# Optimization experiments

Measured on AMD Instinct MI355X. Metric: run time of the kernel, lower is better.

## Reference

```python
import jax, jax.numpy as jnp
import numpy as np

N = 100000
E = 1600000
IN_C = 128
HID = 32
HEADS = 4
NUM_CLASSES = 16
NEG_SLOPE = 0.2


def setup_inputs() -> dict:
    key = jax.random.key(0)
    ks = jax.random.split(key, 10)
    x = jax.random.normal(ks[0], (N, IN_C), dtype=jnp.float32)
    edge_index = jax.random.randint(ks[1], (2, E), 0, N, dtype=jnp.int32)
    s1 = 1.0 / np.sqrt(IN_C)
    s2 = 1.0 / np.sqrt(HID * HEADS)
    W1 = jax.random.normal(ks[2], (IN_C, HEADS * HID), dtype=jnp.float32) * s1
    att_src1 = jax.random.normal(ks[3], (HEADS, HID), dtype=jnp.float32) * s1
    att_dst1 = jax.random.normal(ks[4], (HEADS, HID), dtype=jnp.float32) * s1
    b1 = jnp.zeros((HEADS * HID,), dtype=jnp.float32)
    W2 = jax.random.normal(ks[5], (HEADS * HID, NUM_CLASSES), dtype=jnp.float32) * s2
    att_src2 = jax.random.normal(ks[6], (1, NUM_CLASSES), dtype=jnp.float32) * s2
    att_dst2 = jax.random.normal(ks[7], (1, NUM_CLASSES), dtype=jnp.float32) * s2
    b2 = jnp.zeros((NUM_CLASSES,), dtype=jnp.float32)
    return {"x": x, "edge_index": edge_index,
            "W1": W1, "att_src1": att_src1, "att_dst1": att_dst1, "b1": b1,
            "W2": W2, "att_src2": att_src2, "att_dst2": att_dst2, "b2": b2}


def _gat_conv(x, src, dst, W, att_src, att_dst, b):
    # PyG GATConv: shared linear for src/dst, additive attention, segment softmax over dst.
    n = x.shape[0]
    H, C = att_src.shape
    h = (x @ W).reshape(n, H, C)                       # [N, H, C]
    a_s = jnp.einsum('nhc,hc->nh', h, att_src)          # [N, H]
    a_d = jnp.einsum('nhc,hc->nh', h, att_dst)          # [N, H]
    e = a_s[src] + a_d[dst]                             # [E, H]
    e = jnp.where(e >= 0, e, NEG_SLOPE * e)             # leaky_relu(0.2)
    # numerically stable segment softmax over destination node groups
    e_max = jax.ops.segment_max(e, dst, num_segments=n)
    e_exp = jnp.exp(e - e_max[dst])
    denom = jax.ops.segment_sum(e_exp, dst, num_segments=n)
    alpha = e_exp / denom[dst]                          # [E, H]
    msg = h[src] * alpha[:, :, None]                    # [E, H, C]
    out = jax.ops.segment_sum(msg, dst, num_segments=n) # [N, H, C]
    return out.reshape(n, H * C) + b


def reference(x, edge_index, W1, att_src1, att_dst1, b1, W2, att_src2, att_dst2, b2):
    n = x.shape[0]
    # add_self_loops=True (PyG default), same augmented edge set for both layers
    loop = jnp.arange(n, dtype=edge_index.dtype)
    src = jnp.concatenate([edge_index[0], loop])
    dst = jnp.concatenate([edge_index[1], loop])
    h = _gat_conv(x, src, dst, W1, att_src1, att_dst1, b1)
    h = jax.nn.elu(h)
    out = _gat_conv(h, src, dst, W2, att_src2, att_dst2, b2)
    return out
```

## Files before the change

### kernel.cpp

```cpp
#include <hip/hip_runtime.h>
#include <hip/hip_bf16.h>
#include <math.h>


typedef unsigned short u16;
typedef unsigned int u32;
typedef __attribute__((ext_vector_type(8))) short bf16x8;
typedef __attribute__((ext_vector_type(4))) float f32x4;

__device__ __forceinline__ float eluf(float v) { return v > 0.f ? v : expm1f(v); }
__device__ __forceinline__ u16 f2bf(float f) {
    u32 u = __float_as_uint(f);
    u += 0x7fff + ((u >> 16) & 1);
    return (u16)(u >> 16);
}
__device__ __forceinline__ float bf2f(u16 u) {
    return __uint_as_float(((u32)u) << 16);
}
__device__ __forceinline__ float expleaky(float e) {
    float m = e >= 0.f ? 1.44269504f : 0.28853901f;
    return exp2f(e * m);
}

__global__ __launch_bounds__(256) void ksetup(
    const float* __restrict__ W1, const float* __restrict__ W2,
    const float* __restrict__ ats2, const float* __restrict__ atd2,
    u16* __restrict__ w1fh, u16* __restrict__ w1fl,
    float* __restrict__ u, float* __restrict__ v, u16* __restrict__ w2tb,
    int* __restrict__ deg, int N)
{
    const int b = blockIdx.x, tid = threadIdx.x;
    if (b < 64) {
        int idx = b * 256 + tid;
        int j = idx & 7, l = (idx >> 3) & 63, q = (idx >> 9) & 3, ct = idx >> 11;
        int k = q * 32 + (l >> 4) * 8 + j;
        int n = ct * 16 + (l & 15);
        float w = W1[k * 128 + n];
        u16 hv = f2bf(w);
        w1fh[idx] = hv;
        w1fl[idx] = f2bf(w - bf2f(hv));
    } else if (b == 64) {
        if (tid < 128) {
            float su = 0.f, sv = 0.f;
            #pragma unroll
            for (int j = 0; j < 16; ++j) {
                float w = W2[tid * 16 + j];
                su = fmaf(w, ats2[j], su);
                sv = fmaf(w, atd2[j], sv);
                w2tb[j * 128 + tid] = f2bf(w);
            }
            u[tid] = su; v[tid] = sv;
        }
    } else {
        int z = (b - 65) * 1024 + tid * 4;
        if (z < N) *(int4*)&deg[z] = make_int4(0, 0, 0, 0);
    }
}

__global__ __launch_bounds__(256) void khist(
    const int* __restrict__ ei, int* __restrict__ deg, int* __restrict__ rank,
    int E)
{
    const int base = blockIdx.x * 2048 + threadIdx.x;
    int dd[8];
    #pragma unroll
    for (int k = 0; k < 8; ++k) {
        int e = base + 256 * k;
        dd[k] = (e < E) ? ei[E + e] : -1;
    }
    int rk[8];
    #pragma unroll
    for (int k = 0; k < 8; ++k)
        if (dd[k] >= 0) rk[k] = atomicAdd(&deg[dd[k]], 1);
    #pragma unroll
    for (int k = 0; k < 8; ++k) {
        int e = base + 256 * k;
        if (e < E) rank[e] = rk[k];
    }
}

#define REPW 40
__global__ __launch_bounds__(256) void kgemm(
    const float* __restrict__ x, const u16* __restrict__ w1fh,
    const u16* __restrict__ w1fl,
    const float* __restrict__ att_s, const float* __restrict__ att_d,
    u16* __restrict__ h1b, float* __restrict__ as1, float* __restrict__ ad1,
    int N, int GB)
{
    __shared__ u16 rep[4][16 * REPW];
    const int tid = threadIdx.x;
    const int wv = tid >> 6, lane = tid & 63;
    const int m = lane & 15, quad = lane >> 4;
    const int h = wv;

    bf16x8 bh[2][4], bl[2][4];
    #pragma unroll
    for (int sub = 0; sub < 2; ++sub) {
        #pragma unroll
        for (int q = 0; q < 4; ++q) {
            const int off = (((2 * h + sub) * 4 + q) * 64 + lane) * 8;
            bh[sub][q] = *(const bf16x8*)&w1fh[off];
            bl[sub][q] = *(const bf16x8*)&w1fl[off];
        }
    }
    #pragma unroll
    for (int sub = 0; sub < 2; ++sub) {
        #pragma unroll
        for (int q = 0; q < 4; ++q) {
            asm volatile("" : "+v"(bh[sub][q]));
            asm volatile("" : "+v"(bl[sub][q]));
        }
    }

    const float cs0 = att_s[h * 32 + m];
    const float cs1 = att_s[h * 32 + 16 + m];
    const float cd0 = att_d[h * 32 + m];
    const float cd1 = att_d[h * 32 + 16 + m];

    u16* myrep = rep[wv];
    const int ntile = (N + 15) >> 4;

    for (int t = blockIdx.x; t < ntile; t += GB) {
        const int r0 = t << 4;
        int arow = r0 + m;
        if (arow >= N) arow = N - 1;
        const float* xr = &x[(size_t)arow * 128 + quad * 8];

        bf16x8 ah[4], al[4];
        #pragma unroll
        for (int q = 0; q < 4; ++q) {
            float4 f0 = *(const float4*)&xr[q * 32];
            float4 f1 = *(const float4*)&xr[q * 32 + 4];
            float fv[8] = {f0.x, f0.y, f0.z, f0.w, f1.x, f1.y, f1.z, f1.w};
            union { u16 us[8]; bf16x8 v; } hh, lu;
            #pragma unroll
            for (int j = 0; j < 8; ++j) {
                u16 hvv = f2bf(fv[j]);
                hh.us[j] = hvv;
                lu.us[j] = f2bf(fv[j] - bf2f(hvv));
            }
            ah[q] = hh.v; al[q] = lu.v;
        }

        f32x4 acc[2];
        #pragma unroll
        for (int sub = 0; sub < 2; ++sub) {
            f32x4 a = {0.f, 0.f, 0.f, 0.f};
            #pragma unroll
            for (int q = 0; q < 4; ++q) {
                a = __builtin_amdgcn_mfma_f32_16x16x32_bf16(ah[q], bh[sub][q], a, 0, 0, 0);
                a = __builtin_amdgcn_mfma_f32_16x16x32_bf16(al[q], bh[sub][q], a, 0, 0, 0);
                a = __builtin_amdgcn_mfma_f32_16x16x32_bf16(ah[q], bl[sub][q], a, 0, 0, 0);
            }
            acc[sub] = a;
        }

        float sp[4], dp[4];
        #pragma unroll
        for (int r = 0; r < 4; ++r) {
            sp[r] = fmaf(acc[0][r], cs0, acc[1][r] * cs1);
            dp[r] = fmaf(acc[0][r], cd0, acc[1][r] * cd1);
        }
        #pragma unroll
        for (int r = 0; r < 4; ++r) {
            sp[r] += __shfl_xor(sp[r], 1); sp[r] += __shfl_xor(sp[r], 2);
            sp[r] += __shfl_xor(sp[r], 4); sp[r] += __shfl_xor(sp[r], 8);
            dp[r] += __shfl_xor(dp[r], 1); dp[r] += __shfl_xor(dp[r], 2);
            dp[r] += __shfl_xor(dp[r], 4); dp[r] += __shfl_xor(dp[r], 8);
        }
        if (m == 0) {
            #pragma unroll
            for (int r = 0; r < 4; ++r) {
                int rr = r0 + quad * 4 + r;
                if (rr < N) {
                    as1[rr * 4 + h] = sp[r];
                    ad1[rr * 4 + h] = dp[r];
                }
            }
        }

        #pragma unroll
        for (int sub = 0; sub < 2; ++sub) {
            #pragma unroll
            for (int r = 0; r < 4; ++r)
                myrep[(quad * 4 + r) * REPW + sub * 16 + m] = f2bf(acc[sub][r]);
        }
        __asm__ __volatile__("s_waitcnt lgkmcnt(0)" ::: "memory");
        __builtin_amdgcn_sched_barrier(0);
        const int rr = lane >> 2, cc = lane & 3;
        uint4 vv = *(const uint4*)&myrep[rr * REPW + cc * 8];
        const int grow = r0 + rr;
        if (grow < N)
            *(uint4*)&h1b[(size_t)grow * 128 + h * 32 + cc * 8] = vv;
    }
}

__global__ __launch_bounds__(256) void kscan1(
    const int* __restrict__ deg, int* __restrict__ rowptr,
    int* __restrict__ bsum, int N)
{
    __shared__ int lds[256];
    const int t = threadIdx.x;
    const int base = blockIdx.x * 1024 + t * 4;
    int v[4];
    int s = 0;
    #pragma unroll
    for (int j = 0; j < 4; ++j) {
        v[j] = (base + j < N) ? deg[base + j] : 0;
        s += v[j];
    }
    lds[t] = s;
    __syncthreads();
    for (int off = 1; off < 256; off <<= 1) {
        int y = (t >= off) ? lds[t - off] : 0;
        __syncthreads();
        lds[t] += y;
        __syncthreads();
    }
    int run = lds[t] - s;
    #pragma unroll
    for (int j = 0; j < 4; ++j) {
        if (base + j < N) rowptr[base + j] = run;
        run += v[j];
    }
    if (t == 255) bsum[blockIdx.x] = lds[255];
}

__global__ __launch_bounds__(128) void kscan2(int* __restrict__ bsum, int NB)
{
    __shared__ int lds[128];
    const int t = threadIdx.x;
    int v = (t < NB) ? bsum[t] : 0;
    lds[t] = v;
    __syncthreads();
    for (int off = 1; off < 128; off <<= 1) {
        int y = (t >= off) ? lds[t - off] : 0;
        __syncthreads();
        lds[t] += y;
        __syncthreads();
    }
    if (t < NB) bsum[t] = lds[t] - v;
}

__global__ __launch_bounds__(256) void kscat(
    const int* __restrict__ ei, const int* __restrict__ rowptr,
    const int* __restrict__ bsum, const int* __restrict__ rank,
    int* __restrict__ colidx, int E)
{
    int e = blockIdx.x * 256 + threadIdx.x;
    if (e >= E) return;
    int s = ei[e], d = ei[E + e];
    colidx[rowptr[d] + bsum[d >> 10] + rank[e]] = s;
}

__global__ __launch_bounds__(256) void kg1(
    const int* __restrict__ rowptr, const int* __restrict__ bsum,
    const int* __restrict__ colidx,
    const u16* __restrict__ h1b, const float* __restrict__ as1,
    const float* __restrict__ ad1, const float* __restrict__ b1,
    const float* __restrict__ u, const float* __restrict__ v,
    u16* __restrict__ x2b, float* __restrict__ as2, float* __restrict__ ad2,
    int N, int E)
{
    const int d = blockIdx.x * 4 + (threadIdx.x >> 6);
    if (d >= N) return;
    const int lane = threadIdx.x & 63;
    const int c = lane * 2;
    const int headB = lane >> 4;
    const int headA = lane & 3;
    const int eA = lane >> 2;

    const float adA = ad1[d * 4 + headA];
    const float wself = expleaky(as1[d * 4 + headB] + ad1[d * 4 + headB]);
    u32 hd = *(const u32*)&h1b[(d << 7) + c];
    float accx = wself * bf2f((u16)hd);
    float accy = wself * bf2f((u16)(hd >> 16));
    float den = wself;

    int i0r = rowptr[d] + bsum[d >> 10];
    int i1r = (d + 1 == N) ? E : rowptr[d + 1] + bsum[(d + 1) >> 10];
    const int i0 = __builtin_amdgcn_readfirstlane(i0r);
    const int i1 = __builtin_amdgcn_readfirstlane(i1r);

    for (int i = i0; i < i1; i += 16) {
        const int nb = min(16, i1 - i);
        const int ii = i + eA;
        const int iic = ii < i1 ? ii : i0;
        int sAv = colidx[iic];
        float wA = expleaky(as1[(sAv << 2) + headA] + adA);
        wA = (ii < i1) ? wA : 0.f;
        int e = 0;
        for (; e + 8 <= nb; e += 8) {
            int s0 = colidx[i + e + 0];
            int s1 = colidx[i + e + 1];
            int s2 = colidx[i + e + 2];
            int s3 = colidx[i + e + 3];
            int s4 = colidx[i + e + 4];
            int s5 = colidx[i + e + 5];
            int s6 = colidx[i + e + 6];
            int s7 = colidx[i + e + 7];
            float w0 = __shfl(wA, ((e + 0) << 2) + headB);
            float w1 = __shfl(wA, ((e + 1) << 2) + headB);
            float w2 = __shfl(wA, ((e + 2) << 2) + headB);
            float w3 = __shfl(wA, ((e + 3) << 2) + headB);
            float w4 = __shfl(wA, ((e + 4) << 2) + headB);
            float w5 = __shfl(wA, ((e + 5) << 2) + headB);
            float w6 = __shfl(wA, ((e + 6) << 2) + headB);
            float w7 = __shfl(wA, ((e + 7) << 2) + headB);
            u32 v0 = *(const u32*)&h1b[(s0 << 7) + c];
            u32 v1 = *(const u32*)&h1b[(s1 << 7) + c];
            u32 v2 = *(const u32*)&h1b[(s2 << 7) + c];
            u32 v3 = *(const u32*)&h1b[(s3 << 7) + c];
            u32 v4 = *(const u32*)&h1b[(s4 << 7) + c];
            u32 v5 = *(const u32*)&h1b[(s5 << 7) + c];
            u32 v6 = *(const u32*)&h1b[(s6 << 7) + c];
            u32 v7 = *(const u32*)&h1b[(s7 << 7) + c];
            accx = fmaf(w0, bf2f((u16)v0), accx); accy = fmaf(w0, bf2f((u16)(v0 >> 16)), accy);
            accx = fmaf(w1, bf2f((u16)v1), accx); accy = fmaf(w1, bf2f((u16)(v1 >> 16)), accy);
            accx = fmaf(w2, bf2f((u16)v2), accx); accy = fmaf(w2, bf2f((u16)(v2 >> 16)), accy);
            accx = fmaf(w3, bf2f((u16)v3), accx); accy = fmaf(w3, bf2f((u16)(v3 >> 16)), accy);
            accx = fmaf(w4, bf2f((u16)v4), accx); accy = fmaf(w4, bf2f((u16)(v4 >> 16)), accy);
            accx = fmaf(w5, bf2f((u16)v5), accx); accy = fmaf(w5, bf2f((u16)(v5 >> 16)), accy);
            accx = fmaf(w6, bf2f((u16)v6), accx); accy = fmaf(w6, bf2f((u16)(v6 >> 16)), accy);
            accx = fmaf(w7, bf2f((u16)v7), accx); accy = fmaf(w7, bf2f((u16)(v7 >> 16)), accy);
            den += ((w0 + w1) + (w2 + w3)) + ((w4 + w5) + (w6 + w7));
        }
        for (; e < nb; ++e) {
            int s = colidx[i + e];
            float w = __shfl(wA, (e << 2) + headB);
            u32 hv = *(const u32*)&h1b[(s << 7) + c];
            accx = fmaf(w, bf2f((u16)hv), accx);
            accy = fmaf(w, bf2f((u16)(hv >> 16)), accy);
            den += w;
        }
    }

    const float inv = 1.f / den;
    const float2 bv = *(const float2*)&b1[c];
    const float x2a = eluf(fmaf(accx, inv, bv.x));
    const float x2c = eluf(fmaf(accy, inv, bv.y));

    u32 pk = ((u32)f2bf(x2c) << 16) | (u32)f2bf(x2a);
    *(u32*)&x2b[(d << 7) + c] = pk;

    const float2 uv = *(const float2*)&u[c];
    const float2 vv = *(const float2*)&v[c];
    float sA = fmaf(x2a, uv.x, x2c * uv.y);
    float sB = fmaf(x2a, vv.x, x2c * vv.y);
    #pragma unroll
    for (int m = 1; m < 64; m <<= 1) {
        sA += __shfl_xor(sA, m);
        sB += __shfl_xor(sB, m);
    }
    if (lane == 0) { as2[d] = sA; ad2[d] = sB; }
}

__global__ __launch_bounds__(256) void kh2(
    const u16* __restrict__ x2b, const u16* __restrict__ w2tb,
    u16* __restrict__ h2b, int N)
{
    const int wv = threadIdx.x >> 6, lane = threadIdx.x & 63;
    const int n0 = blockIdx.x * 64 + wv * 16;
    if (n0 >= N) return;
    const int m = lane & 15;
    const int kq = lane >> 4;
    bf16x8 bfr[4];
    #pragma unroll
    for (int q = 0; q < 4; ++q)
        bfr[q] = *(const bf16x8*)&w2tb[m * 128 + q * 32 + kq * 8];

    int ar = n0 + m;
    if (ar >= N) ar = N - 1;
    const u16* arow = &x2b[((size_t)ar << 7) + kq * 8];
    f32x4 acc = {0.f, 0.f, 0.f, 0.f};
    #pragma unroll
    for (int q = 0; q < 4; ++q) {
        bf16x8 af = *(const bf16x8*)&arow[q * 32];
        acc = __builtin_amdgcn_mfma_f32_16x16x32_bf16(af, bfr[q], acc, 0, 0, 0);
    }
    #pragma unroll
    for (int r = 0; r < 4; ++r) {
        int rr = n0 + kq * 4 + r;
        if (rr < N) h2b[((size_t)rr << 4) + m] = f2bf(acc[r]);
    }
}

__global__ __launch_bounds__(256) void kg2(
    const int* __restrict__ rowptr, const int* __restrict__ bsum,
    const int* __restrict__ colidx,
    const u16* __restrict__ h2b, const float* __restrict__ as2,
    const float* __restrict__ ad2, const float* __restrict__ b2,
    float* __restrict__ out, int N, int E)
{
    const int d = blockIdx.x * 4 + (threadIdx.x >> 6);
    if (d >= N) return;
    const int lane = threadIdx.x & 63;
    const int ch = lane & 7, g = lane >> 3;

    const float ad_d = ad2[d];
    float acc0 = 0.f, acc1 = 0.f, den = 0.f;
    int i0r = rowptr[d] + bsum[d >> 10];
    int i1r = (d + 1 == N) ? E : rowptr[d + 1] + bsum[(d + 1) >> 10];
    const int i0 = __builtin_amdgcn_readfirstlane(i0r);
    const int i1 = __builtin_amdgcn_readfirstlane(i1r);

    for (int i = i0; i < i1; i += 64) {
        const int nb = min(64, i1 - i);
        const int idx = i + lane;
        const int idxc = idx < i1 ? idx : i0;
        int sA = colidx[idxc];
        float wA = expleaky(as2[sA] + ad_d);
        wA = (idx < i1) ? wA : 0.f;
        const int kU = (nb + 7) >> 3;
        for (int k = 0; k < kU; ++k) {
            int e = g + 8 * k;
            int ec = e < nb ? e : 0;
            float w = __shfl(wA, ec);
            int s = __shfl(sA, ec);
            if (e >= nb) w = 0.f;
            u32 hv = *(const u32*)&h2b[(s << 4) + ch * 2];
            acc0 = fmaf(w, bf2f((u16)hv), acc0);
            acc1 = fmaf(w, bf2f((u16)(hv >> 16)), acc1);
            den += w;
        }
    }
    acc0 += __shfl_xor(acc0, 8); acc0 += __shfl_xor(acc0, 16); acc0 += __shfl_xor(acc0, 32);
    acc1 += __shfl_xor(acc1, 8); acc1 += __shfl_xor(acc1, 16); acc1 += __shfl_xor(acc1, 32);
    den  += __shfl_xor(den, 8);  den  += __shfl_xor(den, 16);  den  += __shfl_xor(den, 32);

    const float wself = expleaky(as2[d] + ad_d);
    u32 hd = *(const u32*)&h2b[(d << 4) + ch * 2];
    acc0 = fmaf(wself, bf2f((u16)hd), acc0);
    acc1 = fmaf(wself, bf2f((u16)(hd >> 16)), acc1);
    den += wself;
    if (g == 0) {
        float2 ov = {acc0 / den + b2[ch * 2], acc1 / den + b2[ch * 2 + 1]};
        *(float2*)&out[(d << 4) + ch * 2] = ov;
    }
}

extern "C" void kernel_launch(void* const* d_in, const int* in_sizes, int n_in,
                              void* d_out, int out_size, void* d_ws, size_t ws_size,
                              hipStream_t stream) {
    const float* x    = (const float*)d_in[0];
    const int*   ei   = (const int*)d_in[1];
    const float* W1   = (const float*)d_in[2];
    const float* ats1 = (const float*)d_in[3];
    const float* atd1 = (const float*)d_in[4];
    const float* b1   = (const float*)d_in[5];
    const float* W2   = (const float*)d_in[6];
    const float* ats2 = (const float*)d_in[7];
    const float* atd2 = (const float*)d_in[8];
    const float* b2   = (const float*)d_in[9];
    float* out = (float*)d_out;
    const int N = in_sizes[0] / 128;
    const int E = in_sizes[1] / 2;

    u16* h1b   = (u16*)d_ws;
    u16* x2b   = h1b + (size_t)N * 128;
    u16* h2b   = x2b + (size_t)N * 128;
    u16* w2tb  = h2b + (size_t)N * 16;
    u16* w1fh  = w2tb + 2048;
    u16* w1fl  = w1fh + 16384;
    float* as1 = (float*)(w1fl + 16384);
    float* ad1 = as1 + (size_t)N * 4;
    float* as2 = ad1 + (size_t)N * 4;
    float* ad2 = as2 + N;
    float* u   = ad2 + N;
    float* v   = u + 128;
    int* deg    = (int*)(v + 128);
    int* rowptr = deg + ((N + 7) & ~3);
    int* bsum   = rowptr + ((N + 7) & ~3);
    int* colidx = bsum + 128;
    int* rank   = colidx + E;

    const int NB = (N + 1023) / 1024;
    const int KB = (E + 2047) / 2048;
    const int ntile = (N + 15) / 16;
    const int GB = (ntile + 3) / 4;

    hipLaunchKernelGGL(ksetup, dim3(65 + NB), dim3(256), 0, stream,
                       W1, W2, ats2, atd2, w1fh, w1fl, u, v, w2tb, deg, N);
    hipLaunchKernelGGL(khist, dim3(KB), dim3(256), 0, stream,
                       ei, deg, rank, E);
    hipLaunchKernelGGL(kgemm, dim3(GB), dim3(256), 0, stream,
                       x, w1fh, w1fl, ats1, atd1, h1b, as1, ad1, N, GB);
    hipLaunchKernelGGL(kscan1, dim3(NB), dim3(256), 0, stream,
                       deg, rowptr, bsum, N);
    hipLaunchKernelGGL(kscan2, dim3(1), dim3(128), 0, stream, bsum, NB);
    hipLaunchKernelGGL(kscat, dim3((E + 255) / 256), dim3(256), 0, stream,
                       ei, rowptr, bsum, rank, colidx, E);
    hipLaunchKernelGGL(kg1, dim3((N + 3) / 4), dim3(256), 0, stream,
                       rowptr, bsum, colidx, h1b, as1, ad1, b1, u, v,
                       x2b, as2, ad2, N, E);
    hipLaunchKernelGGL(kh2, dim3((N + 63) / 64), dim3(256), 0, stream,
                       x2b, w2tb, h2b, N);
    hipLaunchKernelGGL(kg2, dim3((N + 3) / 4), dim3(256), 0, stream,
                       rowptr, bsum, colidx, h2b, as2, ad2, b2, out, N, E);
}
```

Baseline: 365.5 us.

## Build CSR via two-level bucketed counting sort instead of global atomics

Replaces the global-atomic degree histogram, rank array, two-level scan and random scatter with a bucketed counting sort. Edges are first counted per 512-node bucket in LDS, then the per-bucket offsets are scanned and the edges are scattered into a staging buffer. A per-bucket kernel then builds rowptr and colidx with LDS histograms and LDS atomics. This targets contended global atomics and scattered writes across the whole colidx array, at the cost of more kernel launches and an extra pass through a staging buffer that reuses the x2b workspace.

```diff
diff --git a/kernel.cpp b/kernel.cpp
--- a/kernel.cpp
+++ b/kernel.cpp
@@ -26,8 +26,7 @@
     const float* __restrict__ W1, const float* __restrict__ W2,
     const float* __restrict__ ats2, const float* __restrict__ atd2,
     u16* __restrict__ w1fh, u16* __restrict__ w1fl,
-    float* __restrict__ u, float* __restrict__ v, u16* __restrict__ w2tb,
-    int* __restrict__ deg, int N)
+    float* __restrict__ u, float* __restrict__ v, u16* __restrict__ w2tb)
 {
     const int b = blockIdx.x, tid = threadIdx.x;
     if (b < 64) {
@@ -39,7 +38,7 @@
         u16 hv = f2bf(w);
         w1fh[idx] = hv;
         w1fl[idx] = f2bf(w - bf2f(hv));
-    } else if (b == 64) {
+    } else {
         if (tid < 128) {
             float su = 0.f, sv = 0.f;
             #pragma unroll
@@ -51,31 +50,133 @@
             }
             u[tid] = su; v[tid] = sv;
         }
-    } else {
-        int z = (b - 65) * 1024 + tid * 4;
-        if (z < N) *(int4*)&deg[z] = make_int4(0, 0, 0, 0);
-    }
-}
-
-__global__ __launch_bounds__(256) void khist(
-    const int* __restrict__ ei, int* __restrict__ deg, int* __restrict__ rank,
-    int E)
-{
-    const int base = blockIdx.x * 2048 + threadIdx.x;
+    }
+}
+
+__global__ __launch_bounds__(256) void kcnt(
+    const int* __restrict__ ei, int* __restrict__ M,
+    int E, int NEB, int NBKT)
+{
+    __shared__ int cnt[256];
+    const int b = blockIdx.x, t = threadIdx.x;
+    cnt[t] = 0;
+    __syncthreads();
+    const int e0 = b * 2048 + t;
     int dd[8];
     #pragma unroll
     for (int k = 0; k < 8; ++k) {
-        int e = base + 256 * k;
+        int e = e0 + 256 * k;
         dd[k] = (e < E) ? ei[E + e] : -1;
     }
-    int rk[8];
     #pragma unroll
     for (int k = 0; k < 8; ++k)
-        if (dd[k] >= 0) rk[k] = atomicAdd(&deg[dd[k]], 1);
+        if (dd[k] >= 0) atomicAdd(&cnt[dd[k] >> 9], 1);
+    __syncthreads();
+    if (t < NBKT) M[t * NEB + b] = cnt[t];
+}
+
+__global__ __launch_bounds__(256) void kofs(
+    int* __restrict__ M, int* __restrict__ tot, int NEB)
+{
+    __shared__ int lds[256];
+    const int bkt = blockIdx.x, t = threadIdx.x;
+    int carry = 0;
+    const int rounds = (NEB + 255) / 256;
+    for (int r = 0; r < rounds; ++r) {
+        int idx = r * 256 + t;
+        int v = (idx < NEB) ? M[bkt * NEB + idx] : 0;
+        lds[t] = v;
+        __syncthreads();
+        for (int off = 1; off < 256; off <<= 1) {
+            int y = (t >= off) ? lds[t - off] : 0;
+            __syncthreads();
+            lds[t] += y;
+            __syncthreads();
+        }
+        if (idx < NEB) M[bkt * NEB + idx] = carry + lds[t] - v;
+        carry += lds[255];
+        __syncthreads();
+    }
+    if (t == 0) tot[bkt] = carry;
+}
+
+__global__ __launch_bounds__(256) void kbase(
+    const int* __restrict__ tot, int* __restrict__ base,
+    int* __restrict__ rowptr, int NBKT, int N, int E)
+{
+    __shared__ int lds[256];
+    const int t = threadIdx.x;
+    int v = (t < NBKT) ? tot[t] : 0;
+    lds[t] = v;
+    __syncthreads();
+    for (int off = 1; off < 256; off <<= 1) {
+        int y = (t >= off) ? lds[t - off] : 0;
+        __syncthreads();
+        lds[t] += y;
+        __syncthreads();
+    }
+    if (t < NBKT) base[t] = lds[t] - v;
+    if (t == 0) { base[NBKT] = E; rowptr[N] = E; }
+}
+
+__global__ __launch_bounds__(256) void kbkt2(
+    const int* __restrict__ ei, const int* __restrict__ M,
+    const int* __restrict__ base, uint2* __restrict__ ebuf,
+    int E, int NEB, int NBKT)
+{
+    __shared__ int boff[256];
+    __shared__ int cur[256];
+    const int b = blockIdx.x, t = threadIdx.x;
+    if (t < NBKT) boff[t] = base[t] + M[t * NEB + b];
+    cur[t] = 0;
+    __syncthreads();
+    const int e0 = b * 2048 + t;
+    int dd[8], ss[8];
     #pragma unroll
     for (int k = 0; k < 8; ++k) {
-        int e = base + 256 * k;
-        if (e < E) rank[e] = rk[k];
+        int e = e0 + 256 * k;
+        if (e < E) { dd[k] = ei[E + e]; ss[k] = ei[e]; } else dd[k] = -1;
+    }
+    #pragma unroll
+    for (int k = 0; k < 8; ++k) {
+        if (dd[k] >= 0) {
+            int bkt = dd[k] >> 9;
+            int lr = atomicAdd(&cur[bkt], 1);
+            ebuf[boff[bkt] + lr] = make_uint2((u32)dd[k], (u32)ss[k]);
+        }
+    }
+}
+
+__global__ __launch_bounds__(512) void kcsr(
+    const uint2* __restrict__ ebuf, const int* __restrict__ base,
+    int* __restrict__ rowptr, int* __restrict__ colidx, int N)
+{
+    __shared__ int hist[512];
+    __shared__ int cur[512];
+    const int k = blockIdx.x, t = threadIdx.x;
+    const int e0 = base[k], e1 = base[k + 1];
+    const int n0 = k << 9;
+    const int nb = min(512, N - n0);
+    hist[t] = 0;
+    __syncthreads();
+    for (int i = e0 + t; i < e1; i += 512)
+        atomicAdd(&hist[ebuf[i].x & 511], 1);
+    __syncthreads();
+    int v = hist[t];
+    for (int off = 1; off < 512; off <<= 1) {
+        int y = (t >= off) ? hist[t - off] : 0;
+        __syncthreads();
+        hist[t] += y;
+        __syncthreads();
+    }
+    int excl = hist[t] - v;
+    cur[t] = excl;
+    if (t < nb) rowptr[n0 + t] = e0 + excl;
+    __syncthreads();
+    for (int i = e0 + t; i < e1; i += 512) {
+        uint2 es = ebuf[i];
+        int r = atomicAdd(&cur[es.x & 511], 1);
+        colidx[e0 + r] = (int)es.y;
     }
 }
 
@@ -195,67 +296,8 @@
     }
 }
 
-__global__ __launch_bounds__(256) void kscan1(
-    const int* __restrict__ deg, int* __restrict__ rowptr,
-    int* __restrict__ bsum, int N)
-{
-    __shared__ int lds[256];
-    const int t = threadIdx.x;
-    const int base = blockIdx.x * 1024 + t * 4;
-    int v[4];
-    int s = 0;
-    #pragma unroll
-    for (int j = 0; j < 4; ++j) {
-        v[j] = (base + j < N) ? deg[base + j] : 0;
-        s += v[j];
-    }
-    lds[t] = s;
-    __syncthreads();
-    for (int off = 1; off < 256; off <<= 1) {
-        int y = (t >= off) ? lds[t - off] : 0;
-        __syncthreads();
-        lds[t] += y;
-        __syncthreads();
-    }
-    int run = lds[t] - s;
-    #pragma unroll
-    for (int j = 0; j < 4; ++j) {
-        if (base + j < N) rowptr[base + j] = run;
-        run += v[j];
-    }
-    if (t == 255) bsum[blockIdx.x] = lds[255];
-}
-
-__global__ __launch_bounds__(128) void kscan2(int* __restrict__ bsum, int NB)
-{
-    __shared__ int lds[128];
-    const int t = threadIdx.x;
-    int v = (t < NB) ? bsum[t] : 0;
-    lds[t] = v;
-    __syncthreads();
-    for (int off = 1; off < 128; off <<= 1) {
-        int y = (t >= off) ? lds[t - off] : 0;
-        __syncthreads();
-        lds[t] += y;
-        __syncthreads();
-    }
-    if (t < NB) bsum[t] = lds[t] - v;
-}
-
-__global__ __launch_bounds__(256) void kscat(
-    const int* __restrict__ ei, const int* __restrict__ rowptr,
-    const int* __restrict__ bsum, const int* __restrict__ rank,
-    int* __restrict__ colidx, int E)
-{
-    int e = blockIdx.x * 256 + threadIdx.x;
-    if (e >= E) return;
-    int s = ei[e], d = ei[E + e];
-    colidx[rowptr[d] + bsum[d >> 10] + rank[e]] = s;
-}
-
 __global__ __launch_bounds__(256) void kg1(
-    const int* __restrict__ rowptr, const int* __restrict__ bsum,
-    const int* __restrict__ colidx,
+    const int* __restrict__ rowptr, const int* __restrict__ colidx,
     const u16* __restrict__ h1b, const float* __restrict__ as1,
     const float* __restrict__ ad1, const float* __restrict__ b1,
     const float* __restrict__ u, const float* __restrict__ v,
@@ -277,8 +319,8 @@
     float accy = wself * bf2f((u16)(hd >> 16));
     float den = wself;
 
-    int i0r = rowptr[d] + bsum[d >> 10];
-    int i1r = (d + 1 == N) ? E : rowptr[d + 1] + bsum[(d + 1) >> 10];
+    int i0r = rowptr[d];
+    int i1r = rowptr[d + 1];
     const int i0 = __builtin_amdgcn_readfirstlane(i0r);
     const int i1 = __builtin_amdgcn_readfirstlane(i1r);
 
@@ -386,8 +428,7 @@
 }
 
 __global__ __launch_bounds__(256) void kg2(
-    const int* __restrict__ rowptr, const int* __restrict__ bsum,
-    const int* __restrict__ colidx,
+    const int* __restrict__ rowptr, const int* __restrict__ colidx,
     const u16* __restrict__ h2b, const float* __restrict__ as2,
     const float* __restrict__ ad2, const float* __restrict__ b2,
     float* __restrict__ out, int N, int E)
@@ -399,8 +440,8 @@
 
     const float ad_d = ad2[d];
     float acc0 = 0.f, acc1 = 0.f, den = 0.f;
-    int i0r = rowptr[d] + bsum[d >> 10];
-    int i1r = (d + 1 == N) ? E : rowptr[d + 1] + bsum[(d + 1) >> 10];
+    int i0r = rowptr[d];
+    int i1r = rowptr[d + 1];
     const int i0 = __builtin_amdgcn_readfirstlane(i0r);
     const int i1 = __builtin_amdgcn_readfirstlane(i1r);
 
@@ -456,6 +497,9 @@
     const int N = in_sizes[0] / 128;
     const int E = in_sizes[1] / 2;
 
+    const int NEB  = (E + 2047) / 2048;
+    const int NBKT = (N + 511) >> 9;
+
     u16* h1b   = (u16*)d_ws;
     u16* x2b   = h1b + (size_t)N * 128;
     u16* h2b   = x2b + (size_t)N * 128;
@@ -468,33 +512,34 @@
     float* ad2 = as2 + N;
     float* u   = ad2 + N;
     float* v   = u + 128;
-    int* deg    = (int*)(v + 128);
-    int* rowptr = deg + ((N + 7) & ~3);
-    int* bsum   = rowptr + ((N + 7) & ~3);
-    int* colidx = bsum + 128;
-    int* rank   = colidx + E;
-
-    const int NB = (N + 1023) / 1024;
-    const int KB = (E + 2047) / 2048;
+    int* rowptr = (int*)(v + 128);
+    int* colidx = rowptr + ((N + 8) & ~3);
+    int* M      = colidx + E;
+    int* tot    = M + (size_t)NBKT * NEB;
+    int* base   = tot + NBKT;
+    uint2* ebuf = (uint2*)x2b;
+
     const int ntile = (N + 15) / 16;
     const int GB = (ntile + 3) / 4;
 
-    hipLaunchKernelGGL(ksetup, dim3(65 + NB), dim3(256), 0, stream,
-                       W1, W2, ats2, atd2, w1fh, w1fl, u, v, w2tb, deg, N);
-    hipLaunchKernelGGL(khist, dim3(KB), dim3(256), 0, stream,
-                       ei, deg, rank, E);
+    hipLaunchKernelGGL(ksetup, dim3(65), dim3(256), 0, stream,
+                       W1, W2, ats2, atd2, w1fh, w1fl, u, v, w2tb);
     hipLaunchKernelGGL(kgemm, dim3(GB), dim3(256), 0, stream,
                        x, w1fh, w1fl, ats1, atd1, h1b, as1, ad1, N, GB);
-    hipLaunchKernelGGL(kscan1, dim3(NB), dim3(256), 0, stream,
-                       deg, rowptr, bsum, N);
-    hipLaunchKernelGGL(kscan2, dim3(1), dim3(128), 0, stream, bsum, NB);
-    hipLaunchKernelGGL(kscat, dim3((E + 255) / 256), dim3(256), 0, stream,
-                       ei, rowptr, bsum, rank, colidx, E);
+    hipLaunchKernelGGL(kcnt, dim3(NEB), dim3(256), 0, stream,
+                       ei, M, E, NEB, NBKT);
+    hipLaunchKernelGGL(kofs, dim3(NBKT), dim3(256), 0, stream, M, tot, NEB);
+    hipLaunchKernelGGL(kbase, dim3(1), dim3(256), 0, stream,
+                       tot, base, rowptr, NBKT, N, E);
+    hipLaunchKernelGGL(kbkt2, dim3(NEB), dim3(256), 0, stream,
+                       ei, M, base, ebuf, E, NEB, NBKT);
+    hipLaunchKernelGGL(kcsr, dim3(NBKT), dim3(512), 0, stream,
+                       ebuf, base, rowptr, colidx, N);
     hipLaunchKernelGGL(kg1, dim3((N + 3) / 4), dim3(256), 0, stream,
-                       rowptr, bsum, colidx, h1b, as1, ad1, b1, u, v,
+                       rowptr, colidx, h1b, as1, ad1, b1, u, v,
                        x2b, as2, ad2, N, E);
     hipLaunchKernelGGL(kh2, dim3((N + 63) / 64), dim3(256), 0, stream,
                        x2b, w2tb, h2b, N);
     hipLaunchKernelGGL(kg2, dim3((N + 3) / 4), dim3(256), 0, stream,
-                       rowptr, bsum, colidx, h2b, as2, ad2, b2, out, N, E);
-}
+                       rowptr, colidx, h2b, as2, ad2, b2, out, N, E);
+}
```

Result: faster. 305.5 us (-16.4%).
